# Performance work log

Hardware: AMD Instinct MI355X
Metric: run time of the kernel (lower is better)

The kernel has to match this reference:

```python
import jax, jax.numpy as jnp
import numpy as np

N_I = 500_000   # 'indivi' nodes (dst)
N_H = 200_000   # 'house' nodes
F_I = 32        # indivi feature dim
F_H = 16        # house feature dim
EF = 8          # edge_attr dim
E1 = 2_000_000  # house->indivi edges
E2 = 2_000_000  # indivi->indivi edges


def setup_inputs() -> dict:
    key = jax.random.key(0)
    ks = jax.random.split(key, 16)
    return {
        "x_indivi": jax.random.normal(ks[0], (N_I, F_I), jnp.float32),
        "x_house": jax.random.normal(ks[1], (N_H, F_H), jnp.float32),
        "edge_attr_h2i": jax.random.normal(ks[2], (E1, EF), jnp.float32),
        "edge_attr_i2i": jax.random.normal(ks[3], (E2, EF), jnp.float32),
        "W_edge_h2i": jax.random.normal(ks[4], (F_H, EF), jnp.float32) * 0.1,
        "b_edge_h2i": jax.random.normal(ks[5], (F_H,), jnp.float32) * 0.1,
        "W_edge_i2i": jax.random.normal(ks[6], (F_I, EF), jnp.float32) * 0.1,
        "b_edge_i2i": jax.random.normal(ks[7], (F_I,), jnp.float32) * 0.1,
        "W_root_h2i": jax.random.normal(ks[8], (1, F_I), jnp.float32) * 0.1,
        "bias_h2i": jax.random.normal(ks[9], (1,), jnp.float32) * 0.1,
        "W_root_i2i": jax.random.normal(ks[10], (1, F_I), jnp.float32) * 0.1,
        "bias_i2i": jax.random.normal(ks[11], (1,), jnp.float32) * 0.1,
        "src_h2i": jax.random.randint(ks[12], (E1,), 0, N_H, jnp.int32),
        "dst_h2i": jax.random.randint(ks[13], (E1,), 0, N_I, jnp.int32),
        "src_i2i": jax.random.randint(ks[14], (E2,), 0, N_I, jnp.int32),
        "dst_i2i": jax.random.randint(ks[15], (E2,), 0, N_I, jnp.int32),
    }


def _nnconv(x_src, x_dst, edge_attr, src, dst, W_edge, b_edge, W_root, bias, num_dst):
    # Edge MLP -> per-edge weight matrix of shape [F_src, out=1], flattened to [E, F_src]
    w = edge_attr @ W_edge.T + b_edge                     # [E, F_src]
    # message_e = x_src[src_e] @ w_e  (out_channels = 1)
    msg = jnp.sum(x_src[src] * w, axis=-1, keepdims=True)  # [E, 1]
    agg = jax.ops.segment_sum(msg, dst, num_segments=num_dst)  # [N_dst, 1]
    # root transform on destination features + bias
    return agg + x_dst @ W_root.T + bias                  # [N_dst, 1]


def reference(x_indivi, x_house, edge_attr_h2i, edge_attr_i2i,
              W_edge_h2i, b_edge_h2i, W_edge_i2i, b_edge_i2i,
              W_root_h2i, bias_h2i, W_root_i2i, bias_i2i,
              src_h2i, dst_h2i, src_i2i, dst_i2i):
    out_h = _nnconv(x_house, x_indivi, edge_attr_h2i, src_h2i, dst_h2i,
                    W_edge_h2i, b_edge_h2i, W_root_h2i, bias_h2i, N_I)
    out_i = _nnconv(x_indivi, x_indivi, edge_attr_i2i, src_i2i, dst_i2i,
                    W_edge_i2i, b_edge_i2i, W_root_i2i, bias_i2i, N_I)
    # HeteroConv(aggr='sum') over the two relations targeting 'indivi'
    return out_h + out_i
```

## Files before the change

kernel.cpp:

```cpp
#include <hip/hip_runtime.h>

#define N_I 500000
#define N_H 200000
#define E1  2000000
#define E2  2000000
#define TOTAL_E (E1 + E2)

#define BSHIFT 12
#define NB 128
#define NBK ((N_I + 4095) / 4096)
#define CHUNK 2048
#define NWG ((TOTAL_E + CHUNK - 1) / CHUNK)
#define WPT 8
#define ITERS (CHUNK / 256)

template<int F, bool ROOT>
__global__ __launch_bounds__(256) void precompute_g(
    const float* __restrict__ x, const float* __restrict__ W, const float* __restrict__ b,
    float* __restrict__ g8, float* __restrict__ gc, int n,
    const float* __restrict__ rW1, const float* __restrict__ rW2,
    const float* __restrict__ rb1, const float* __restrict__ rb2,
    float* __restrict__ out)
{
    __shared__ float Wf[F * 8];
    __shared__ float bv[F];
    __shared__ float wr[F];

    for (int i = threadIdx.x; i < F * 8; i += 256) Wf[i] = W[i];
    if (threadIdx.x < F) {
        bv[threadIdx.x] = b[threadIdx.x];
        if (ROOT) wr[threadIdx.x] = rW1[threadIdx.x] + rW2[threadIdx.x];
    }
    __syncthreads();

    int nid = blockIdx.x * 256 + threadIdx.x;
    if (nid >= n) return;

    float xv[F];
    const float4* xp = (const float4*)(x + (size_t)nid * F);
    #pragma unroll
    for (int q = 0; q < F / 4; q++) {
        float4 v = xp[q];
        xv[q*4+0] = v.x; xv[q*4+1] = v.y; xv[q*4+2] = v.z; xv[q*4+3] = v.w;
    }

    float acc[9];
    #pragma unroll
    for (int k = 0; k < 9; k++) acc[k] = 0.f;

    #pragma unroll
    for (int j = 0; j < F; j++) {
        float4 w0 = *(const float4*)(Wf + j * 8);
        float4 w1 = *(const float4*)(Wf + j * 8 + 4);
        float xj = xv[j];
        acc[0] = fmaf(xj, w0.x, acc[0]);
        acc[1] = fmaf(xj, w0.y, acc[1]);
        acc[2] = fmaf(xj, w0.z, acc[2]);
        acc[3] = fmaf(xj, w0.w, acc[3]);
        acc[4] = fmaf(xj, w1.x, acc[4]);
        acc[5] = fmaf(xj, w1.y, acc[5]);
        acc[6] = fmaf(xj, w1.z, acc[6]);
        acc[7] = fmaf(xj, w1.w, acc[7]);
        acc[8] = fmaf(xj, bv[j], acc[8]);
    }

    float4* gp = (float4*)(g8 + (size_t)nid * 8);
    gp[0] = make_float4(acc[0], acc[1], acc[2], acc[3]);
    gp[1] = make_float4(acc[4], acc[5], acc[6], acc[7]);
    gc[nid] = acc[8];

    if (ROOT) {
        float r = rb1[0] + rb2[0];
        #pragma unroll
        for (int j = 0; j < F; j++) r = fmaf(xv[j], wr[j], r);
        out[nid] = r;
    }
}

__global__ __launch_bounds__(256) void hist_kernel(
    const int* __restrict__ dst1, const int* __restrict__ dst2,
    int* __restrict__ H)
{
    __shared__ int hist[NB];
    if (threadIdx.x < NB) hist[threadIdx.x] = 0;
    __syncthreads();

    int base = blockIdx.x * CHUNK;
    #pragma unroll
    for (int it = 0; it < ITERS; ++it) {
        int t = base + it * 256 + threadIdx.x;
        if (t < TOTAL_E) {
            int d = (t < E1) ? dst1[t] : dst2[t - E1];
            atomicAdd(&hist[d >> BSHIFT], 1);
        }
    }
    __syncthreads();
    if (threadIdx.x < NB) H[blockIdx.x * NB + threadIdx.x] = hist[threadIdx.x];
}

__global__ __launch_bounds__(256) void scan_cols_kernel(int* __restrict__ H,
                                                        int* __restrict__ total)
{
    __shared__ int sums[256];
    int b = blockIdx.x;
    int tid = threadIdx.x;

    int vals[WPT];
    int s = 0;
    #pragma unroll
    for (int k = 0; k < WPT; k++) {
        int w = tid * WPT + k;
        vals[k] = (w < NWG) ? H[w * NB + b] : 0;
        s += vals[k];
    }
    sums[tid] = s;
    __syncthreads();
    for (int off = 1; off < 256; off <<= 1) {
        int t = (tid >= off) ? sums[tid - off] : 0;
        __syncthreads();
        sums[tid] += t;
        __syncthreads();
    }
    int run = sums[tid] - s;
    #pragma unroll
    for (int k = 0; k < WPT; k++) {
        int w = tid * WPT + k;
        if (w < NWG) H[w * NB + b] = run;
        run += vals[k];
    }
    if (tid == 255) total[b] = sums[255];
}

__global__ __launch_bounds__(128) void scan_base_kernel(const int* __restrict__ total,
                                                        int* __restrict__ base)
{
    __shared__ int v[NB];
    int tid = threadIdx.x;
    int orig = total[tid];
    v[tid] = orig;
    __syncthreads();
    for (int off = 1; off < NB; off <<= 1) {
        int t = (tid >= off) ? v[tid - off] : 0;
        __syncthreads();
        v[tid] += t;
        __syncthreads();
    }
    base[tid] = v[tid] - orig;
}

__device__ __forceinline__ void compute_msgs8(
    int tid, int ebase,
    const int* __restrict__ src, const int* __restrict__ dst,
    const float* __restrict__ ea, const float4* __restrict__ g8,
    const float* __restrict__ gc,
    int* dloc, float* mloc)
{
    int sl[ITERS];
    #pragma unroll
    for (int it = 0; it < ITERS; ++it) {
        int e = ebase + it * 256 + tid;
        sl[it] = src[e];
        dloc[it] = dst[e];
    }
    #pragma unroll
    for (int h = 0; h < 2; ++h) {
        float4 ga[4], gb[4], a0[4], a1[4];
        float gv[4];
        #pragma unroll
        for (int k = 0; k < 4; ++k) {
            int it = h * 4 + k;
            int e = ebase + it * 256 + tid;
            int s = sl[it];
            ga[k] = g8[(size_t)s * 2];
            gb[k] = g8[(size_t)s * 2 + 1];
            gv[k] = gc[s];
            const float4* ap = (const float4*)(ea + (size_t)e * 8);
            a0[k] = ap[0];
            a1[k] = ap[1];
        }
        #pragma unroll
        for (int k = 0; k < 4; ++k) {
            float m = gv[k];
            m = fmaf(a0[k].x, ga[k].x, m);
            m = fmaf(a0[k].y, ga[k].y, m);
            m = fmaf(a0[k].z, ga[k].z, m);
            m = fmaf(a0[k].w, ga[k].w, m);
            m = fmaf(a1[k].x, gb[k].x, m);
            m = fmaf(a1[k].y, gb[k].y, m);
            m = fmaf(a1[k].z, gb[k].z, m);
            m = fmaf(a1[k].w, gb[k].w, m);
            mloc[h * 4 + k] = m;
        }
    }
}

__global__ __launch_bounds__(256) void scatter_fused_kernel(
    const int* __restrict__ src1, const int* __restrict__ dst1,
    const float* __restrict__ ea1, const float4* __restrict__ g8_1, const float* __restrict__ gc_1,
    const int* __restrict__ src2, const int* __restrict__ dst2,
    const float* __restrict__ ea2, const float4* __restrict__ g8_2, const float* __restrict__ gc_2,
    const int* __restrict__ H, const int* __restrict__ base,
    float* __restrict__ msgs_out, unsigned short* __restrict__ lidx_out)
{
    __shared__ int cnt[NB];
    __shared__ int sv[NB];
    __shared__ int gbase[NB];
    __shared__ unsigned int lu[CHUNK];
    __shared__ float lm[CHUNK];

    int tid = threadIdx.x;
    if (tid < NB) cnt[tid] = 0;
    __syncthreads();

    int cbase = blockIdx.x * CHUNK;
    int dloc[ITERS];
    float mloc[ITERS];

    if (cbase + CHUNK <= E1) {
        compute_msgs8(tid, cbase, src1, dst1, ea1, g8_1, gc_1, dloc, mloc);
    } else if (cbase >= E1 && cbase + CHUNK <= TOTAL_E) {
        compute_msgs8(tid, cbase - E1, src2, dst2, ea2, g8_2, gc_2, dloc, mloc);
    } else {
        #pragma unroll
        for (int it = 0; it < ITERS; ++it) {
            int t = cbase + it * 256 + tid;
            int d = -1; float m = 0.f;
            if (t < TOTAL_E) {
                const int* srcp; const int* dstp; const float* eap;
                const float4* g8p; const float* gcp; int e;
                if (t < E1) { e = t;      srcp = src1; dstp = dst1; eap = ea1; g8p = g8_1; gcp = gc_1; }
                else        { e = t - E1; srcp = src2; dstp = dst2; eap = ea2; g8p = g8_2; gcp = gc_2; }
                int s = srcp[e];
                d = dstp[e];
                float4 ga = g8p[(size_t)s * 2];
                float4 gb = g8p[(size_t)s * 2 + 1];
                const float4* ap = (const float4*)(eap + (size_t)e * 8);
                float4 a0 = ap[0];
                float4 a1 = ap[1];
                m = gcp[s];
                m = fmaf(a0.x, ga.x, m);
                m = fmaf(a0.y, ga.y, m);
                m = fmaf(a0.z, ga.z, m);
                m = fmaf(a0.w, ga.w, m);
                m = fmaf(a1.x, gb.x, m);
                m = fmaf(a1.y, gb.y, m);
                m = fmaf(a1.z, gb.z, m);
                m = fmaf(a1.w, gb.w, m);
            }
            dloc[it] = d; mloc[it] = m;
        }
    }

    #pragma unroll
    for (int it = 0; it < ITERS; ++it)
        if (dloc[it] >= 0) atomicAdd(&cnt[dloc[it] >> BSHIFT], 1);
    __syncthreads();

    int myc = 0;
    if (tid < NB) { myc = cnt[tid]; sv[tid] = myc; }
    __syncthreads();
    for (int off = 1; off < NB; off <<= 1) {
        int t = (tid < NB && tid >= off) ? sv[tid - off] : 0;
        __syncthreads();
        if (tid < NB) sv[tid] += t;
        __syncthreads();
    }
    if (tid < NB) {
        int loff = sv[tid] - myc;
        gbase[tid] = H[blockIdx.x * NB + tid] + base[tid] - loff;
        cnt[tid] = loff;
    }
    __syncthreads();

    #pragma unroll
    for (int it = 0; it < ITERS; ++it) {
        int d = dloc[it];
        if (d >= 0) {
            int b = d >> BSHIFT;
            int slot = atomicAdd(&cnt[b], 1);
            lu[slot] = ((unsigned)b << BSHIFT) | (unsigned)(d & 4095);
            lm[slot] = mloc[it];
        }
    }
    __syncthreads();

    int nvalid = TOTAL_E - cbase;
    if (nvalid > CHUNK) nvalid = CHUNK;
    for (int i = tid; i < nvalid; i += 256) {
        unsigned u = lu[i];
        int b = (int)(u >> BSHIFT);
        int g = gbase[b] + i;
        msgs_out[g] = lm[i];
        lidx_out[g] = (unsigned short)(u & 4095u);
    }
}

__global__ __launch_bounds__(512) void reduce_kernel(
    const float* __restrict__ msgs, const unsigned short* __restrict__ lidx,
    const int* __restrict__ base, const int* __restrict__ total,
    float* __restrict__ part)
{
    __shared__ float acc[4096];
    for (int i = threadIdx.x; i < 4096; i += 512) acc[i] = 0.f;
    __syncthreads();

    int b = blockIdx.x >> 2;
    int k = blockIdx.x & 3;
    int start = base[b];
    int cnt = total[b];
    int q = (cnt + 3) >> 2;
    int s0 = k * q;
    int s1 = s0 + q; if (s1 > cnt) s1 = cnt;

    for (int i = s0 + threadIdx.x; i < s1; i += 512) {
        atomicAdd(&acc[lidx[start + i]], msgs[start + i]);
    }
    __syncthreads();

    float* dp = part + (size_t)blockIdx.x * 4096;
    for (int i = threadIdx.x; i < 4096; i += 512) dp[i] = acc[i];
}

__global__ __launch_bounds__(256) void merge_kernel(
    const float* __restrict__ part, float* __restrict__ out)
{
    int n = blockIdx.x * 256 + threadIdx.x;
    if (n < N_I) {
        int b = n >> BSHIFT;
        int i = n & 4095;
        const float* p = part + (size_t)b * 4 * 4096 + i;
        out[n] += (p[0] + p[4096]) + (p[8192] + p[12288]);
    }
}

__global__ __launch_bounds__(256) void edge_kernel_atomic(
    const int* __restrict__ src1, const int* __restrict__ dst1,
    const float* __restrict__ ea1, const float4* __restrict__ g8_1, const float* __restrict__ gc_1,
    const int* __restrict__ src2, const int* __restrict__ dst2,
    const float* __restrict__ ea2, const float4* __restrict__ g8_2, const float* __restrict__ gc_2,
    float* __restrict__ out)
{
    int t = blockIdx.x * 256 + threadIdx.x;
    if (t >= TOTAL_E) return;
    const int* srcp; const int* dstp; const float* eap;
    const float4* g8p; const float* gcp; int e;
    if (t < E1) { e = t;      srcp = src1; dstp = dst1; eap = ea1; g8p = g8_1; gcp = gc_1; }
    else        { e = t - E1; srcp = src2; dstp = dst2; eap = ea2; g8p = g8_2; gcp = gc_2; }
    int s = srcp[e];
    int d = dstp[e];
    float4 ga = g8p[(size_t)s * 2];
    float4 gb = g8p[(size_t)s * 2 + 1];
    const float4* ap = (const float4*)(eap + (size_t)e * 8);
    float4 a0 = ap[0];
    float4 a1 = ap[1];
    float m = gcp[s];
    m = fmaf(a0.x, ga.x, m);
    m = fmaf(a0.y, ga.y, m);
    m = fmaf(a0.z, ga.z, m);
    m = fmaf(a0.w, ga.w, m);
    m = fmaf(a1.x, gb.x, m);
    m = fmaf(a1.y, gb.y, m);
    m = fmaf(a1.z, gb.z, m);
    m = fmaf(a1.w, gb.w, m);
    atomicAdd(out + d, m);
}

extern "C" void kernel_launch(void* const* d_in, const int* in_sizes, int n_in,
                              void* d_out, int out_size, void* d_ws, size_t ws_size,
                              hipStream_t stream) {
    const float* x_i  = (const float*)d_in[0];
    const float* x_h  = (const float*)d_in[1];
    const float* ea_h = (const float*)d_in[2];
    const float* ea_i = (const float*)d_in[3];
    const float* We_h = (const float*)d_in[4];
    const float* be_h = (const float*)d_in[5];
    const float* We_i = (const float*)d_in[6];
    const float* be_i = (const float*)d_in[7];
    const float* Wr_h = (const float*)d_in[8];
    const float* br_h = (const float*)d_in[9];
    const float* Wr_i = (const float*)d_in[10];
    const float* br_i = (const float*)d_in[11];
    const int* src_h = (const int*)d_in[12];
    const int* dst_h = (const int*)d_in[13];
    const int* src_i = (const int*)d_in[14];
    const int* dst_i = (const int*)d_in[15];

    float* out = (float*)d_out;

    char* ws = (char*)d_ws;
    float* g8_i = (float*)ws;
    float* g8_h = (float*)(ws + 16000000);
    float* gc_i = (float*)(ws + 22400000);
    float* gc_h = (float*)(ws + 24400000);
    float* msgs = (float*)(ws + 25200000);
    unsigned short* lidx = (unsigned short*)(ws + 41200000);
    float* part = (float*)ws;
    int*   H    = (int*)(ws + 49200000);
    int*   tot  = (int*)(ws + 50200448);
    int*   bas  = (int*)(ws + 50201472);
    const size_t WS_NEEDED = 50201984;

    precompute_g<16, false><<<(N_H + 255) / 256, 256, 0, stream>>>(
        x_h, We_h, be_h, g8_h, gc_h, N_H, nullptr, nullptr, nullptr, nullptr, nullptr);
    precompute_g<32, true><<<(N_I + 255) / 256, 256, 0, stream>>>(
        x_i, We_i, be_i, g8_i, gc_i, N_I, Wr_h, Wr_i, br_h, br_i, out);

    if (ws_size >= WS_NEEDED) {
        hist_kernel<<<NWG, 256, 0, stream>>>(dst_h, dst_i, H);
        scan_cols_kernel<<<NB, 256, 0, stream>>>(H, tot);
        scan_base_kernel<<<1, NB, 0, stream>>>(tot, bas);
        scatter_fused_kernel<<<NWG, 256, 0, stream>>>(
            src_h, dst_h, ea_h, (const float4*)g8_h, gc_h,
            src_i, dst_i, ea_i, (const float4*)g8_i, gc_i,
            H, bas, msgs, lidx);
        reduce_kernel<<<NBK * 4, 512, 0, stream>>>(msgs, lidx, bas, tot, part);
        merge_kernel<<<(N_I + 255) / 256, 256, 0, stream>>>(part, out);
    } else {
        edge_kernel_atomic<<<(TOTAL_E + 255) / 256, 256, 0, stream>>>(
            src_h, dst_h, ea_h, (const float4*)g8_h, gc_h,
            src_i, dst_i, ea_i, (const float4*)g8_i, gc_i, out);
    }
}
```

Baseline: 372.4 us.

## Store per-node g in fp16, add nontemporal loads, fuse merge into atomic reduce

Per-node precomputed projections g8 and gc are now stored as fp16, which halves the gather traffic in the edge scatter pass. Streaming loads and stores of edge arrays, indices and messages switch to nontemporal hints. The separate merge kernel and its partial buffer are removed, and each reduce block now atomically adds its shared-memory bucket sums straight into the output. This trades fp16 rounding of intermediate node values and some global atomics for fewer bytes moved and one fewer launch.

Result: no change. 366.0 us (-1.7%).

```diff
diff --git a/kernel.cpp b/kernel.cpp
--- a/kernel.cpp
+++ b/kernel.cpp
@@ -14,10 +14,12 @@
 #define WPT 8
 #define ITERS (CHUNK / 256)
 
+typedef float f4 __attribute__((ext_vector_type(4)));
+
 template<int F, bool ROOT>
 __global__ __launch_bounds__(256) void precompute_g(
     const float* __restrict__ x, const float* __restrict__ W, const float* __restrict__ b,
-    float* __restrict__ g8, float* __restrict__ gc, int n,
+    uint4* __restrict__ g8, _Float16* __restrict__ gc, int n,
     const float* __restrict__ rW1, const float* __restrict__ rW2,
     const float* __restrict__ rb1, const float* __restrict__ rb2,
     float* __restrict__ out)
@@ -37,11 +39,11 @@
     if (nid >= n) return;
 
     float xv[F];
-    const float4* xp = (const float4*)(x + (size_t)nid * F);
+    const f4* xp = (const f4*)(x + (size_t)nid * F);
     #pragma unroll
     for (int q = 0; q < F / 4; q++) {
-        float4 v = xp[q];
-        xv[q*4+0] = v.x; xv[q*4+1] = v.y; xv[q*4+2] = v.z; xv[q*4+3] = v.w;
+        f4 v = __builtin_nontemporal_load(xp + q);
+        xv[q*4+0] = v[0]; xv[q*4+1] = v[1]; xv[q*4+2] = v[2]; xv[q*4+3] = v[3];
     }
 
     float acc[9];
@@ -64,10 +66,11 @@
         acc[8] = fmaf(xj, bv[j], acc[8]);
     }
 
-    float4* gp = (float4*)(g8 + (size_t)nid * 8);
-    gp[0] = make_float4(acc[0], acc[1], acc[2], acc[3]);
-    gp[1] = make_float4(acc[4], acc[5], acc[6], acc[7]);
-    gc[nid] = acc[8];
+    union { _Float16 h[8]; uint4 u; } pk;
+    #pragma unroll
+    for (int k = 0; k < 8; k++) pk.h[k] = (_Float16)acc[k];
+    g8[nid] = pk.u;
+    gc[nid] = (_Float16)acc[8];
 
     if (ROOT) {
         float r = rb1[0] + rb2[0];
@@ -90,7 +93,8 @@
     for (int it = 0; it < ITERS; ++it) {
         int t = base + it * 256 + threadIdx.x;
         if (t < TOTAL_E) {
-            int d = (t < E1) ? dst1[t] : dst2[t - E1];
+            int d = (t < E1) ? __builtin_nontemporal_load(&dst1[t])
+                             : __builtin_nontemporal_load(&dst2[t - E1]);
             atomicAdd(&hist[d >> BSHIFT], 1);
         }
     }
@@ -148,57 +152,60 @@
     base[tid] = v[tid] - orig;
 }
 
+__device__ __forceinline__ float msg_dot(uint4 gu, f4 a0, f4 a1, float base) {
+    union { uint4 u; _Float16 h[8]; } pk; pk.u = gu;
+    float m = base;
+    m = fmaf((float)pk.h[0], a0[0], m);
+    m = fmaf((float)pk.h[1], a0[1], m);
+    m = fmaf((float)pk.h[2], a0[2], m);
+    m = fmaf((float)pk.h[3], a0[3], m);
+    m = fmaf((float)pk.h[4], a1[0], m);
+    m = fmaf((float)pk.h[5], a1[1], m);
+    m = fmaf((float)pk.h[6], a1[2], m);
+    m = fmaf((float)pk.h[7], a1[3], m);
+    return m;
+}
+
 __device__ __forceinline__ void compute_msgs8(
     int tid, int ebase,
     const int* __restrict__ src, const int* __restrict__ dst,
-    const float* __restrict__ ea, const float4* __restrict__ g8,
-    const float* __restrict__ gc,
+    const float* __restrict__ ea, const uint4* __restrict__ g8,
+    const _Float16* __restrict__ gc,
     int* dloc, float* mloc)
 {
     int sl[ITERS];
     #pragma unroll
     for (int it = 0; it < ITERS; ++it) {
         int e = ebase + it * 256 + tid;
-        sl[it] = src[e];
-        dloc[it] = dst[e];
+        sl[it] = __builtin_nontemporal_load(&src[e]);
+        dloc[it] = __builtin_nontemporal_load(&dst[e]);
     }
     #pragma unroll
     for (int h = 0; h < 2; ++h) {
-        float4 ga[4], gb[4], a0[4], a1[4];
+        uint4 g[4]; f4 a0[4], a1[4];
         float gv[4];
         #pragma unroll
         for (int k = 0; k < 4; ++k) {
             int it = h * 4 + k;
             int e = ebase + it * 256 + tid;
             int s = sl[it];
-            ga[k] = g8[(size_t)s * 2];
-            gb[k] = g8[(size_t)s * 2 + 1];
-            gv[k] = gc[s];
-            const float4* ap = (const float4*)(ea + (size_t)e * 8);
-            a0[k] = ap[0];
-            a1[k] = ap[1];
+            g[k] = g8[s];
+            gv[k] = (float)gc[s];
+            const f4* ap = (const f4*)(ea + (size_t)e * 8);
+            a0[k] = __builtin_nontemporal_load(ap);
+            a1[k] = __builtin_nontemporal_load(ap + 1);
         }
         #pragma unroll
-        for (int k = 0; k < 4; ++k) {
-            float m = gv[k];
-            m = fmaf(a0[k].x, ga[k].x, m);
-            m = fmaf(a0[k].y, ga[k].y, m);
-            m = fmaf(a0[k].z, ga[k].z, m);
-            m = fmaf(a0[k].w, ga[k].w, m);
-            m = fmaf(a1[k].x, gb[k].x, m);
-            m = fmaf(a1[k].y, gb[k].y, m);
-            m = fmaf(a1[k].z, gb[k].z, m);
-            m = fmaf(a1[k].w, gb[k].w, m);
-            mloc[h * 4 + k] = m;
-        }
+        for (int k = 0; k < 4; ++k)
+            mloc[h * 4 + k] = msg_dot(g[k], a0[k], a1[k], gv[k]);
     }
 }
 
 __global__ __launch_bounds__(256) void scatter_fused_kernel(
     const int* __restrict__ src1, const int* __restrict__ dst1,
-    const float* __restrict__ ea1, const float4* __restrict__ g8_1, const float* __restrict__ gc_1,
+    const float* __restrict__ ea1, const uint4* __restrict__ g8_1, const _Float16* __restrict__ gc_1,
     const int* __restrict__ src2, const int* __restrict__ dst2,
-    const float* __restrict__ ea2, const float4* __restrict__ g8_2, const float* __restrict__ gc_2,
+    const float* __restrict__ ea2, const uint4* __restrict__ g8_2, const _Float16* __restrict__ gc_2,
     const int* __restrict__ H, const int* __restrict__ base,
     float* __restrict__ msgs_out, unsigned short* __restrict__ lidx_out)
 {
@@ -227,25 +234,16 @@
             int d = -1; float m = 0.f;
             if (t < TOTAL_E) {
                 const int* srcp; const int* dstp; const float* eap;
-                const float4* g8p; const float* gcp; int e;
+                const uint4* g8p; const _Float16* gcp; int e;
                 if (t < E1) { e = t;      srcp = src1; dstp = dst1; eap = ea1; g8p = g8_1; gcp = gc_1; }
                 else        { e = t - E1; srcp = src2; dstp = dst2; eap = ea2; g8p = g8_2; gcp = gc_2; }
                 int s = srcp[e];
                 d = dstp[e];
-                float4 ga = g8p[(size_t)s * 2];
-                float4 gb = g8p[(size_t)s * 2 + 1];
-                const float4* ap = (const float4*)(eap + (size_t)e * 8);
-                float4 a0 = ap[0];
-                float4 a1 = ap[1];
-                m = gcp[s];
-                m = fmaf(a0.x, ga.x, m);
-                m = fmaf(a0.y, ga.y, m);
-                m = fmaf(a0.z, ga.z, m);
-                m = fmaf(a0.w, ga.w, m);
-                m = fmaf(a1.x, gb.x, m);
-                m = fmaf(a1.y, gb.y, m);
-                m = fmaf(a1.z, gb.z, m);
-                m = fmaf(a1.w, gb.w, m);
+                uint4 gu = g8p[s];
+                const f4* ap = (const f4*)(eap + (size_t)e * 8);
+                f4 a0 = ap[0];
+                f4 a1 = ap[1];
+                m = msg_dot(gu, a0, a1, (float)gcp[s]);
             }
             dloc[it] = d; mloc[it] = m;
         }
@@ -290,15 +288,15 @@
         unsigned u = lu[i];
         int b = (int)(u >> BSHIFT);
         int g = gbase[b] + i;
-        msgs_out[g] = lm[i];
-        lidx_out[g] = (unsigned short)(u & 4095u);
-    }
-}
-
-__global__ __launch_bounds__(512) void reduce_kernel(
+        __builtin_nontemporal_store(lm[i], &msgs_out[g]);
+        __builtin_nontemporal_store((unsigned short)(u & 4095u), &lidx_out[g]);
+    }
+}
+
+__global__ __launch_bounds__(512) void reduce_atomic_kernel(
     const float* __restrict__ msgs, const unsigned short* __restrict__ lidx,
     const int* __restrict__ base, const int* __restrict__ total,
-    float* __restrict__ part)
+    float* __restrict__ out)
 {
     __shared__ float acc[4096];
     for (int i = threadIdx.x; i < 4096; i += 512) acc[i] = 0.f;
@@ -313,55 +311,40 @@
     int s1 = s0 + q; if (s1 > cnt) s1 = cnt;
 
     for (int i = s0 + threadIdx.x; i < s1; i += 512) {
-        atomicAdd(&acc[lidx[start + i]], msgs[start + i]);
-    }
-    __syncthreads();
-
-    float* dp = part + (size_t)blockIdx.x * 4096;
-    for (int i = threadIdx.x; i < 4096; i += 512) dp[i] = acc[i];
-}
-
-__global__ __launch_bounds__(256) void merge_kernel(
-    const float* __restrict__ part, float* __restrict__ out)
-{
-    int n = blockIdx.x * 256 + threadIdx.x;
-    if (n < N_I) {
-        int b = n >> BSHIFT;
-        int i = n & 4095;
-        const float* p = part + (size_t)b * 4 * 4096 + i;
-        out[n] += (p[0] + p[4096]) + (p[8192] + p[12288]);
+        unsigned short li = __builtin_nontemporal_load(&lidx[start + i]);
+        float mv = __builtin_nontemporal_load(&msgs[start + i]);
+        atomicAdd(&acc[li], mv);
+    }
+    __syncthreads();
+
+    int node0 = b << BSHIFT;
+    for (int i = threadIdx.x; i < 4096; i += 512) {
+        float v = acc[i];
+        int n = node0 + i;
+        if (v != 0.f && n < N_I) atomicAdd(out + n, v);
     }
 }
 
 __global__ __launch_bounds__(256) void edge_kernel_atomic(
     const int* __restrict__ src1, const int* __restrict__ dst1,
-    const float* __restrict__ ea1, const float4* __restrict__ g8_1, const float* __restrict__ gc_1,
+    const float* __restrict__ ea1, const uint4* __restrict__ g8_1, const _Float16* __restrict__ gc_1,
     const int* __restrict__ src2, const int* __restrict__ dst2,
-    const float* __restrict__ ea2, const float4* __restrict__ g8_2, const float* __restrict__ gc_2,
+    const float* __restrict__ ea2, const uint4* __restrict__ g8_2, const _Float16* __restrict__ gc_2,
     float* __restrict__ out)
 {
     int t = blockIdx.x * 256 + threadIdx.x;
     if (t >= TOTAL_E) return;
     const int* srcp; const int* dstp; const float* eap;
-    const float4* g8p; const float* gcp; int e;
+    const uint4* g8p; const _Float16* gcp; int e;
     if (t < E1) { e = t;      srcp = src1; dstp = dst1; eap = ea1; g8p = g8_1; gcp = gc_1; }
     else        { e = t - E1; srcp = src2; dstp = dst2; eap = ea2; g8p = g8_2; gcp = gc_2; }
     int s = srcp[e];
     int d = dstp[e];
-    float4 ga = g8p[(size_t)s * 2];
-    float4 gb = g8p[(size_t)s * 2 + 1];
-    const float4* ap = (const float4*)(eap + (size_t)e * 8);
-    float4 a0 = ap[0];
-    float4 a1 = ap[1];
-    float m = gcp[s];
-    m = fmaf(a0.x, ga.x, m);
-    m = fmaf(a0.y, ga.y, m);
-    m = fmaf(a0.z, ga.z, m);
-    m = fmaf(a0.w, ga.w, m);
-    m = fmaf(a1.x, gb.x, m);
-    m = fmaf(a1.y, gb.y, m);
-    m = fmaf(a1.z, gb.z, m);
-    m = fmaf(a1.w, gb.w, m);
+    uint4 gu = g8p[s];
+    const f4* ap = (const f4*)(eap + (size_t)e * 8);
+    f4 a0 = ap[0];
+    f4 a1 = ap[1];
+    float m = msg_dot(gu, a0, a1, (float)gcp[s]);
     atomicAdd(out + d, m);
 }
 
@@ -388,17 +371,16 @@
     float* out = (float*)d_out;
 
     char* ws = (char*)d_ws;
-    float* g8_i = (float*)ws;
-    float* g8_h = (float*)(ws + 16000000);
-    float* gc_i = (float*)(ws + 22400000);
-    float* gc_h = (float*)(ws + 24400000);
-    float* msgs = (float*)(ws + 25200000);
-    unsigned short* lidx = (unsigned short*)(ws + 41200000);
-    float* part = (float*)ws;
-    int*   H    = (int*)(ws + 49200000);
-    int*   tot  = (int*)(ws + 50200448);
-    int*   bas  = (int*)(ws + 50201472);
-    const size_t WS_NEEDED = 50201984;
+    uint4*    g8_i = (uint4*)ws;
+    uint4*    g8_h = (uint4*)(ws + 8000000);
+    _Float16* gc_i = (_Float16*)(ws + 11200000);
+    _Float16* gc_h = (_Float16*)(ws + 12200000);
+    float*    msgs = (float*)(ws + 12800000);
+    unsigned short* lidx = (unsigned short*)(ws + 28800000);
+    int*      H    = (int*)(ws + 36800000);
+    int*      tot  = (int*)(ws + 37800448);
+    int*      bas  = (int*)(ws + 37800960);
+    const size_t WS_NEEDED = 37801472;
 
     precompute_g<16, false><<<(N_H + 255) / 256, 256, 0, stream>>>(
         x_h, We_h, be_h, g8_h, gc_h, N_H, nullptr, nullptr, nullptr, nullptr, nullptr);
@@ -410,14 +392,13 @@
         scan_cols_kernel<<<NB, 256, 0, stream>>>(H, tot);
         scan_base_kernel<<<1, NB, 0, stream>>>(tot, bas);
         scatter_fused_kernel<<<NWG, 256, 0, stream>>>(
-            src_h, dst_h, ea_h, (const float4*)g8_h, gc_h,
-            src_i, dst_i, ea_i, (const float4*)g8_i, gc_i,
+            src_h, dst_h, ea_h, g8_h, gc_h,
+            src_i, dst_i, ea_i, g8_i, gc_i,
             H, bas, msgs, lidx);
-        reduce_kernel<<<NBK * 4, 512, 0, stream>>>(msgs, lidx, bas, tot, part);
-        merge_kernel<<<(N_I + 255) / 256, 256, 0, stream>>>(part, out);
+        reduce_atomic_kernel<<<NBK * 4, 512, 0, stream>>>(msgs, lidx, bas, tot, out);
     } else {
         edge_kernel_atomic<<<(TOTAL_E + 255) / 256, 256, 0, stream>>>(
-            src_h, dst_h, ea_h, (const float4*)g8_h, gc_h,
-            src_i, dst_i, ea_i, (const float4*)g8_i, gc_i, out);
-    }
-}
+            src_h, dst_h, ea_h, g8_h, gc_h,
+            src_i, dst_i, ea_i, g8_i, gc_i, out);
+    }
+}
```
